# Kernel optimization log

Hardware: AMD Instinct MI355X
Metric: run time of the kernel (lower is better)

The kernel has to match this reference:

```python
import jax, jax.numpy as jnp
import numpy as np
from jax import lax

NEG = -1e30  # finite stand-in for -inf so logaddexp grads stay finite


def setup_inputs() -> dict:
    key = jax.random.key(0)
    k1, k2, k3, k4, k5 = jax.random.split(key, 5)
    B, T, L, S = 16, 2048, 256, 8
    return {
        "emissions": jax.random.normal(k1, (B, T, S), dtype=jnp.float32),
        "transition": jax.random.normal(k2, (S, S), dtype=jnp.float32),
        "bos": jax.random.normal(k3, (S,), dtype=jnp.float32),
        "eos": jax.random.normal(k4, (S,), dtype=jnp.float32),
        "lengths": jnp.full((B,), T, dtype=jnp.int32),
        "targets": jax.random.randint(k5, (B, L), 0, 4, dtype=jnp.int32),
        "target_lengths": jnp.full((B,), L, dtype=jnp.int32),
    }


def _den_logz(em, lengths, transition, bos, eos):
    # Exact log-semiring forward over the fully-connected 8-state denominator CRF graph
    # (the limit of k2.intersect_dense_pruned(...).get_tot_scores(log_semiring=True)).
    B, T, S = em.shape
    alpha0 = bos[None, :] + em[:, 0, :]  # (B,S)

    def step(alpha, em_t):
        a = jax.nn.logsumexp(alpha[:, :, None] + transition[None, :, :], axis=1) + em_t
        return a, a

    _, alphas = lax.scan(step, alpha0, jnp.swapaxes(em, 0, 1)[1:])  # (T-1,B,S)
    alphas = jnp.concatenate([alpha0[None], alphas], axis=0)  # (T,B,S)
    fin = alphas[lengths - 1, jnp.arange(B)]  # (B,S) alpha at last valid frame
    return jax.nn.logsumexp(fin + eos[None, :], axis=-1)


def _num_logz(em, lengths, targets, target_lengths, transition, bos, eos):
    # Forward over the target-constrained enter/extend lattice: symbol u must be
    # entered (state targets[u]) exactly once, optionally extended (state targets[u]+4),
    # then the path moves monotonically to symbol u+1.
    B, T, S = em.shape
    L = targets.shape[1]
    b_idx = jnp.arange(B)
    es = targets          # enter-state ids, (B,L)
    xs = targets + 4      # extend-state ids, (B,L)

    t_xx = transition[xs, xs]  # extend_u -> extend_u
    t_ex = transition[es, xs]  # enter_u  -> extend_u
    prev_e = jnp.concatenate([es[:, :1], es[:, :-1]], axis=1)
    prev_x = jnp.concatenate([xs[:, :1], xs[:, :-1]], axis=1)
    t_ee = transition[prev_e, es]  # enter_{u-1}  -> enter_u
    t_xe = transition[prev_x, es]  # extend_{u-1} -> enter_u

    a_e0 = jnp.full((B, L), NEG, dtype=em.dtype)
    a_e0 = a_e0.at[:, 0].set(bos[es[:, 0]] + em[b_idx, 0, es[:, 0]])
    a_x0 = jnp.full((B, L), NEG, dtype=em.dtype)

    def shift(a):  # a[:, u-1], NEG at u=0
        return jnp.concatenate([jnp.full((B, 1), NEG, dtype=a.dtype), a[:, :-1]], axis=1)

    def step(carry, em_t):
        a_e, a_x = carry
        em_e = jnp.take_along_axis(em_t, es, axis=1)  # (B,L)
        em_x = jnp.take_along_axis(em_t, xs, axis=1)
        new_e = em_e + jnp.logaddexp(shift(a_e) + t_ee, shift(a_x) + t_xe)
        new_x = em_x + jnp.logaddexp(a_e + t_ex, a_x + t_xx)
        return (new_e, new_x), (new_e, new_x)

    _, (ae, ax) = lax.scan(step, (a_e0, a_x0), jnp.swapaxes(em, 0, 1)[1:])
    ae = jnp.concatenate([a_e0[None], ae], axis=0)  # (T,B,L)
    ax = jnp.concatenate([a_x0[None], ax], axis=0)
    fin_e = ae[lengths - 1, b_idx]  # (B,L)
    fin_x = ax[lengths - 1, b_idx]
    u = target_lengths - 1
    fe = fin_e[b_idx, u] + eos[es[b_idx, u]]
    fx = fin_x[b_idx, u] + eos[xs[b_idx, u]]
    return jnp.logaddexp(fe, fx)  # (B,)


def reference(emissions, transition, bos, eos, lengths, targets, target_lengths):
    em = emissions.astype(jnp.float32)
    logz_den = _den_logz(em, lengths, transition, bos, eos)
    logz_num = _num_logz(em, lengths, targets, target_lengths, transition, bos, eos)
    # all samples valid by construction (lengths > 0, 0 < target_len <= length)
    return jnp.mean(logz_den - logz_num)
```

## Files before the change

### kernel.cpp

```cpp
#include <hip/hip_runtime.h>
#include <math.h>


#define LOG2E 1.4426950408889634f
#define LN2   0.69314718055994531f
#define CTL_WSHL1  0x130
#define CTL_WSHR1  0x138
#define CTL_ROR(r) (0x120 + (r))

#define AST(p, v) __hip_atomic_store((p), (v), __ATOMIC_RELAXED, __HIP_MEMORY_SCOPE_AGENT)
#define ALD(p)    __hip_atomic_load((p), __ATOMIC_RELAXED, __HIP_MEMORY_SCOPE_AGENT)

template <int CTRL>
__device__ __forceinline__ float fdpp(float x) {
    return __int_as_float(__builtin_amdgcn_update_dpp(
        0, __float_as_int(x), CTRL, 0xF, 0xF, true));
}
template <int CTRL>
__device__ __forceinline__ int idpp(int x) {
    return __builtin_amdgcn_update_dpp(0, x, CTRL, 0xF, 0xF, true);
}

__device__ __forceinline__ void pin() {
#if __has_builtin(__builtin_amdgcn_sched_barrier)
    __builtin_amdgcn_sched_barrier(0);
#else
    asm volatile("" ::: "memory");
#endif
}

__device__ __forceinline__ float fexp2(float x) {
#if __has_builtin(__builtin_amdgcn_exp2f)
    return __builtin_amdgcn_exp2f(x);
#else
    return exp2f(x);
#endif
}
__device__ __forceinline__ float flog2(float x) {
#if __has_builtin(__builtin_amdgcn_logf)
    return __builtin_amdgcn_logf(x);
#else
    return __log2f(x);
#endif
}
__device__ __forceinline__ float lse2(float a, float b) {
    float m = fmaxf(a, b);
    float d = fminf(a, b) - m;
    return m + flog2(1.0f + fexp2(d));
}

struct NumC { float tee[4], txe[4], tex[4], txx[4]; };

__device__ __forceinline__ void numf_step(const float2* p, float* E, float* X,
                                          float teeF, float txeF, const NumC& c) {
    float nbE = fdpp<CTL_WSHR1>(E[3]);
    float nbX = fdpp<CTL_WSHR1>(X[3]);
    float nE0 = p[0].x * fmaf(nbE,  teeF,     nbX  * txeF);
    float nE1 = p[1].x * fmaf(E[0], c.tee[1], X[0] * c.txe[1]);
    float nE2 = p[2].x * fmaf(E[1], c.tee[2], X[1] * c.txe[2]);
    float nE3 = p[3].x * fmaf(E[2], c.tee[3], X[2] * c.txe[3]);
    float nX0 = p[0].y * fmaf(E[0], c.tex[0], X[0] * c.txx[0]);
    float nX1 = p[1].y * fmaf(E[1], c.tex[1], X[1] * c.txx[1]);
    float nX2 = p[2].y * fmaf(E[2], c.tex[2], X[2] * c.txx[2]);
    float nX3 = p[3].y * fmaf(E[3], c.tex[3], X[3] * c.txx[3]);
    E[0] = nE0; E[1] = nE1; E[2] = nE2; E[3] = nE3;
    X[0] = nX0; X[1] = nX1; X[2] = nX2; X[3] = nX3;
}

__device__ __forceinline__ void numf_boundary(float* E, float* X, int& s,
                                              float& teeF, float& txeF,
                                              int lane, const NumC& c) {
    float m = fmaxf(fmaxf(fmaxf(E[0], E[1]), fmaxf(E[2], E[3])),
                    fmaxf(fmaxf(X[0], X[1]), fmaxf(X[2], X[3])));
    const bool live = (m > 0.0f);
    const int ex = live ? ((int)(__float_as_uint(m) >> 23) - 126) : 0;
    s += ex;
    const int bs = idpp<CTL_WSHR1>(s);
    if (!live) s = bs;
    int d = (lane == 0) ? 0 : (bs - s);
    const int extra = (d > 30) ? d : 0;
    s += extra; d -= extra;
    const float fsc = ldexpf(1.0f, -(ex + extra));
#pragma unroll
    for (int k = 0; k < 4; ++k) { E[k] *= fsc; X[k] *= fsc; }
    const float fs0 = (lane == 0) ? 0.0f : ldexpf(1.0f, d);
    teeF = c.tee[0] * fs0;
    txeF = c.txe[0] * fs0;
}

__device__ __forceinline__ void numb_step(const float2* p, float* bE, float* bX,
                                          const float* tex, const float* txx,
                                          const float* teeN, const float* txeN,
                                          float teeN3F, float txeN3F) {
    float mm0 = p[0].x * bE[0];
    float mm1 = p[1].x * bE[1];
    float mm2 = p[2].x * bE[2];
    float mm3 = p[3].x * bE[3];
    float m10 = p[0].y * bX[0];
    float m11 = p[1].y * bX[1];
    float m12 = p[2].y * bX[2];
    float m13 = p[3].y * bX[3];
    float mup = fdpp<CTL_WSHL1>(mm0);
    float nE0 = fmaf(tex[0], m10, teeN[0] * mm1);
    float nE1 = fmaf(tex[1], m11, teeN[1] * mm2);
    float nE2 = fmaf(tex[2], m12, teeN[2] * mm3);
    float nE3 = fmaf(tex[3], m13, teeN3F   * mup);
    float nX0 = fmaf(txx[0], m10, txeN[0] * mm1);
    float nX1 = fmaf(txx[1], m11, txeN[1] * mm2);
    float nX2 = fmaf(txx[2], m12, txeN[2] * mm3);
    float nX3 = fmaf(txx[3], m13, txeN3F   * mup);
    bE[0] = nE0; bE[1] = nE1; bE[2] = nE2; bE[3] = nE3;
    bX[0] = nX0; bX[1] = nX1; bX[2] = nX2; bX[3] = nX3;
}

__device__ __forceinline__ void numb_boundary(float* bE, float* bX, int& s,
                                              float& teeN3F, float& txeN3F,
                                              int lane, float teeN3, float txeN3) {
    float m = fmaxf(fmaxf(fmaxf(bE[0], bE[1]), fmaxf(bE[2], bE[3])),
                    fmaxf(fmaxf(bX[0], bX[1]), fmaxf(bX[2], bX[3])));
    const bool live = (m > 0.0f);
    const int ex = live ? ((int)(__float_as_uint(m) >> 23) - 126) : 0;
    s += ex;
    const int bs = idpp<CTL_WSHL1>(s);
    if (!live) s = bs;
    int d = (lane == 63) ? 0 : (bs - s);
    const int extra = (d > 30) ? d : 0;
    s += extra; d -= extra;
    const float fsc = ldexpf(1.0f, -(ex + extra));
#pragma unroll
    for (int k = 0; k < 4; ++k) { bE[k] *= fsc; bX[k] *= fsc; }
    const float fs = (lane == 63) ? 0.0f : ldexpf(1.0f, d);
    teeN3F = teeN3 * fs;
    txeN3F = txeN3 * fs;
}

__device__ __forceinline__ void steps4_fwd(const float4 buf[4][2], float* E, float* X,
                                           float teeF, float txeF, const NumC& c) {
#pragma unroll
    for (int q = 0; q < 4; ++q) {
        float2 p[4];
#pragma unroll
        for (int k = 0; k < 4; ++k) {
            const float4 v = buf[k][q >> 1];
            p[k] = (q & 1) ? make_float2(v.z, v.w) : make_float2(v.x, v.y);
        }
        numf_step(p, E, X, teeF, txeF, c);
    }
}
__device__ __forceinline__ void steps4_bwd(const float4 buf[4][2], float* bE, float* bX,
                                           const float* tex, const float* txx,
                                           const float* teeN, const float* txeN,
                                           float teeN3F, float txeN3F) {
#pragma unroll
    for (int q = 0; q < 4; ++q) {
        const int h = 1 - (q >> 1);
        float2 p[4];
#pragma unroll
        for (int k = 0; k < 4; ++k) {
            const float4 v = buf[k][h];
            p[k] = (q & 1) ? make_float2(v.x, v.y) : make_float2(v.z, v.w);
        }
        numb_step(p, bE, bX, tex, txx, teeN, txeN, teeN3F, txeN3F);
    }
}

__device__ __forceinline__ float denf_step(float al, float emt, const float* Tr) {
    float v1 = fdpp<CTL_ROR(1)>(al);
    float v2 = fdpp<CTL_ROR(2)>(al);
    float v3 = fdpp<CTL_ROR(3)>(al);
    float v4 = fdpp<CTL_ROR(4)>(al);
    float v5 = fdpp<CTL_ROR(5)>(al);
    float v6 = fdpp<CTL_ROR(6)>(al);
    float v7 = fdpp<CTL_ROR(7)>(al);
    float q0 = fmaf(v1, Tr[1], al * Tr[0]);
    float q1 = fmaf(v3, Tr[3], v2 * Tr[2]);
    float q2 = fmaf(v5, Tr[5], v4 * Tr[4]);
    float q3 = fmaf(v7, Tr[7], v6 * Tr[6]);
    return ((q0 + q1) + (q2 + q3)) * emt;
}
__device__ __forceinline__ float denb_step(float al, float emt, const float* TrB) {
    float g  = al * emt;
    float v1 = fdpp<CTL_ROR(7)>(g);
    float v2 = fdpp<CTL_ROR(6)>(g);
    float v3 = fdpp<CTL_ROR(5)>(g);
    float v4 = fdpp<CTL_ROR(4)>(g);
    float v5 = fdpp<CTL_ROR(3)>(g);
    float v6 = fdpp<CTL_ROR(2)>(g);
    float v7 = fdpp<CTL_ROR(1)>(g);
    float q0 = fmaf(v1, TrB[1], g * TrB[0]);
    float q1 = fmaf(v3, TrB[3], v2 * TrB[2]);
    float q2 = fmaf(v5, TrB[5], v4 * TrB[4]);
    float q3 = fmaf(v7, TrB[7], v6 * TrB[6]);
    return (q0 + q1) + (q2 + q3);
}
__device__ __forceinline__ int den_renorm(float& al) {
    float mm = fmaxf(al, fdpp<CTL_ROR(4)>(al));
    mm = fmaxf(mm, fdpp<CTL_ROR(2)>(mm));
    mm = fmaxf(mm, fdpp<CTL_ROR(1)>(mm));
    const int ex = (int)(__float_as_uint(mm) >> 23) - 126;
    al = ldexpf(al, -ex);
    return ex;
}

extern "C" __global__ void __launch_bounds__(128)
crf_fused(const float* __restrict__ em, const float* __restrict__ trans,
          const float* __restrict__ bos, const float* __restrict__ eos,
          const int* __restrict__ lengths, const int* __restrict__ targets,
          const int* __restrict__ tlens,
          float* __restrict__ ws, float* __restrict__ out,
          int B, int T, int S, int L)
{
    extern __shared__ float sm[];
    const int bid  = blockIdx.x;
    const int tid  = threadIdx.x;
    const int lane = tid & 63;
    const int wv   = tid >> 6;
    const int half = S >> 1;
    const int role = bid / B;
    const int b    = bid % B;
    const float* gem = em + (size_t)b * T * S;
    const int len = lengths[b];
    const int tm  = (len - 1) >> 1;
    const int P2  = T + 2;
    const int Th2 = P2 >> 1;

    float* NF  = ws + 16 + (size_t)b * 576;
    float* NB  = ws + 16 + (size_t)B * 576 + (size_t)b * 576;
    float* DEN = ws + 16 + (size_t)(2 * B) * 576;
    int* ticket = (int*)ws;

    if (role < 2) {
        float2* s2 = (float2*)sm;
        for (int t = tid; t < T; t += 128) {
            const float4* gr = (const float4*)(gem + t * S);
            float4 a = gr[0], c4 = gr[1];
            s2[0 * P2 + t] = make_float2(fexp2(a.x * LOG2E), fexp2(c4.x * LOG2E));
            s2[1 * P2 + t] = make_float2(fexp2(a.y * LOG2E), fexp2(c4.y * LOG2E));
            s2[2 * P2 + t] = make_float2(fexp2(a.z * LOG2E), fexp2(c4.z * LOG2E));
            s2[3 * P2 + t] = make_float2(fexp2(a.w * LOG2E), fexp2(c4.w * LOG2E));
        }
    } else {
        for (int t = tid; t < T; t += 128) {
            const float4* gr = (const float4*)(gem + t * S);
            float4 a = gr[0], c4 = gr[1];
            float4 w0, w1;
            w0.x = fexp2(a.x * LOG2E); w0.y = fexp2(c4.x * LOG2E);
            w0.z = fexp2(a.y * LOG2E); w0.w = fexp2(c4.y * LOG2E);
            w1.x = fexp2(a.z * LOG2E); w1.y = fexp2(c4.z * LOG2E);
            w1.z = fexp2(a.w * LOG2E); w1.w = fexp2(c4.w * LOG2E);
            ((float4*)sm)[t * 2]     = w0;
            ((float4*)sm)[t * 2 + 1] = w1;
        }
    }
    __syncthreads();

    if (role == 0 && wv == 0) {
        const float2* s2 = (const float2*)sm;
        const float4* s4 = (const float4*)sm;
        const int u0 = lane * 4;
        int e[4], ep[4];
        const int base = b * L;
#pragma unroll
        for (int k = 0; k < 4; ++k) {
            int u = u0 + k;
            e[k] = targets[base + ((u < L) ? u : (L - 1))];
        }
        ep[0] = (u0 > 0) ? targets[base + u0 - 1] : e[0];
        ep[1] = e[0]; ep[2] = e[1]; ep[3] = e[2];
        NumC c;
#pragma unroll
        for (int k = 0; k < 4; ++k) {
            c.tee[k] = fexp2(trans[ep[k] * S + e[k]] * LOG2E);
            c.txe[k] = fexp2(trans[(ep[k] + half) * S + e[k]] * LOG2E);
            c.tex[k] = fexp2(trans[e[k] * S + e[k] + half] * LOG2E);
            c.txx[k] = fexp2(trans[(e[k] + half) * S + e[k] + half] * LOG2E);
        }
        float E[4] = {0.f,0.f,0.f,0.f}, X[4] = {0.f,0.f,0.f,0.f};
        int s = 0;
        if (lane == 0) E[0] = fexp2(bos[e[0]] * LOG2E) * s2[e[0] * P2].x;
        float teeF = (lane == 0) ? 0.0f : c.tee[0];
        float txeF = (lane == 0) ? 0.0f : c.txe[0];

        int t0 = 1;
        while (t0 <= tm && (t0 & 1)) {
            float2 p[4];
#pragma unroll
            for (int k = 0; k < 4; ++k) p[k] = s2[e[k] * P2 + t0];
            numf_step(p, E, X, teeF, txeF, c);
            ++t0;
        }
        if (t0 + 7 <= tm) {
            float4 A[4][2], Bf[4][2];
#pragma unroll
            for (int k = 0; k < 4; ++k) {
                A[k][0] = s4[e[k] * Th2 + (t0 >> 1)];
                A[k][1] = s4[e[k] * Th2 + ((t0 + 2) >> 1)];
            }
            pin();
            while (t0 + 7 <= tm) {
#pragma unroll
                for (int k = 0; k < 4; ++k) {
                    Bf[k][0] = s4[e[k] * Th2 + ((t0 + 4) >> 1)];
                    Bf[k][1] = s4[e[k] * Th2 + ((t0 + 6) >> 1)];
                }
                pin();
                steps4_fwd(A, E, X, teeF, txeF, c);
#pragma unroll
                for (int k = 0; k < 4; ++k) {
                    A[k][0] = s4[e[k] * Th2 + ((t0 + 8) >> 1)];
                    A[k][1] = s4[e[k] * Th2 + ((t0 + 10) >> 1)];
                }
                pin();
                steps4_fwd(Bf, E, X, teeF, txeF, c);
                numf_boundary(E, X, s, teeF, txeF, lane, c);
                t0 += 8;
            }
        }
        while (t0 <= tm) {
            float2 p[4];
#pragma unroll
            for (int k = 0; k < 4; ++k) p[k] = s2[e[k] * P2 + t0];
            numf_step(p, E, X, teeF, txeF, c);
            ++t0;
        }
#pragma unroll
        for (int k = 0; k < 4; ++k) {
            AST(&NF[lane * 8 + k],     E[k]);
            AST(&NF[lane * 8 + 4 + k], X[k]);
        }
        AST(&NF[512 + lane], __int_as_float(s));
    } else if (role == 1 && wv == 0) {
        const float2* s2 = (const float2*)sm;
        const float4* s4 = (const float4*)sm;
        const int u0 = lane * 4;
        int e[5];
        const int base = b * L;
#pragma unroll
        for (int k = 0; k < 5; ++k) {
            int u = u0 + k;
            e[k] = targets[base + ((u < L) ? u : (L - 1))];
        }
        float tex[4], txx[4], teeN[4], txeN[4];
#pragma unroll
        for (int k = 0; k < 4; ++k) {
            tex[k]  = fexp2(trans[e[k] * S + e[k] + half] * LOG2E);
            txx[k]  = fexp2(trans[(e[k] + half) * S + e[k] + half] * LOG2E);
            teeN[k] = fexp2(trans[e[k] * S + e[k + 1]] * LOG2E);
            txeN[k] = fexp2(trans[(e[k] + half) * S + e[k + 1]] * LOG2E);
        }
        if (lane == 63) { teeN[3] = 0.0f; txeN[3] = 0.0f; }
        float bE[4] = {0.f,0.f,0.f,0.f}, bX[4] = {0.f,0.f,0.f,0.f};
        const int uf = tlens[b] - 1;
        if (lane == (uf >> 2)) {
            const int kf = uf & 3;
            bE[kf] = fexp2(eos[e[kf]] * LOG2E);
            bX[kf] = fexp2(eos[e[kf] + half] * LOG2E);
        }
        int s = 0;
        float teeN3F = teeN[3], txeN3F = txeN[3];

        int t1 = len - 1;
        const int tlo = tm + 1;
        while (t1 >= tlo && !(t1 & 1)) {
            float2 p[4];
#pragma unroll
            for (int k = 0; k < 4; ++k) p[k] = s2[e[k] * P2 + t1];
            numb_step(p, bE, bX, tex, txx, teeN, txeN, teeN3F, txeN3F);
            --t1;
        }
        if (t1 - 7 >= tlo) {
            float4 A[4][2], Bf[4][2];
#pragma unroll
            for (int k = 0; k < 4; ++k) {
                A[k][0] = s4[e[k] * Th2 + ((t1 - 3) >> 1)];
                A[k][1] = s4[e[k] * Th2 + ((t1 - 1) >> 1)];
            }
            pin();
            while (t1 - 7 >= tlo) {
#pragma unroll
                for (int k = 0; k < 4; ++k) {
                    Bf[k][0] = s4[e[k] * Th2 + ((t1 - 7) >> 1)];
                    Bf[k][1] = s4[e[k] * Th2 + ((t1 - 5) >> 1)];
                }
                pin();
                steps4_bwd(A, bE, bX, tex, txx, teeN, txeN, teeN3F, txeN3F);
                const int ta = (t1 - 11 > 0) ? (t1 - 11) : 0;
#pragma unroll
                for (int k = 0; k < 4; ++k) {
                    A[k][0] = s4[e[k] * Th2 + (ta >> 1)];
                    A[k][1] = s4[e[k] * Th2 + ((ta + 2) >> 1)];
                }
                pin();
                steps4_bwd(Bf, bE, bX, tex, txx, teeN, txeN, teeN3F, txeN3F);
                numb_boundary(bE, bX, s, teeN3F, txeN3F, lane, teeN[3], txeN[3]);
                t1 -= 8;
            }
        }
        while (t1 >= tlo) {
            float2 p[4];
#pragma unroll
            for (int k = 0; k < 4; ++k) p[k] = s2[e[k] * P2 + t1];
            numb_step(p, bE, bX, tex, txx, teeN, txeN, teeN3F, txeN3F);
            --t1;
        }
#pragma unroll
        for (int k = 0; k < 4; ++k) {
            AST(&NB[lane * 8 + k],     bE[k]);
            AST(&NB[lane * 8 + 4 + k], bX[k]);
        }
        AST(&NB[512 + lane], __int_as_float(s));
    } else if (role == 2) {
        float* denF  = sm + T * 8 + 16;
        float* denB  = denF + 8;
        int*   denFs = (int*)(denB + 8);
        int*   denBs = denFs + 8;
        const int j  = lane & 7;
        const int jj = ((j & 3) << 1) + (j >> 2);
        if (wv == 0) {
            float Tr[8];
#pragma unroll
            for (int r = 0; r < 8; ++r)
                Tr[r] = fexp2(trans[((j - r) & 7) * S + j] * LOG2E);
            float al = fexp2(bos[j] * LOG2E) * sm[jj];
            int sc = 0;
            int t = 1;
            while (t + 3 <= tm) {
                float c0 = sm[t * 8 + jj];
                float c1 = sm[(t + 1) * 8 + jj];
                float c2 = sm[(t + 2) * 8 + jj];
                float c3 = sm[(t + 3) * 8 + jj];
                pin();
                al = denf_step(al, c0, Tr);
                al = denf_step(al, c1, Tr);
                al = denf_step(al, c2, Tr);
                al = denf_step(al, c3, Tr);
                sc += den_renorm(al);
                t += 4;
            }
            while (t <= tm) { al = denf_step(al, sm[t * 8 + jj], Tr); ++t; }
            if (lane < 8) { denF[j] = al; denFs[j] = sc; }
        } else {
            float TrB[8];
#pragma unroll
            for (int r = 0; r < 8; ++r)
                TrB[r] = fexp2(trans[j * S + ((j + r) & 7)] * LOG2E);
            float al = fexp2(eos[j] * LOG2E);
            int sc = 0;
            int t = len - 1;
            const int tlo = tm + 1;
            while (t - 3 >= tlo) {
                float c0 = sm[t * 8 + jj];
                float c1 = sm[(t - 1) * 8 + jj];
                float c2 = sm[(t - 2) * 8 + jj];
                float c3 = sm[(t - 3) * 8 + jj];
                pin();
                al = denb_step(al, c0, TrB);
                al = denb_step(al, c1, TrB);
                al = denb_step(al, c2, TrB);
                al = denb_step(al, c3, TrB);
                sc += den_renorm(al);
                t -= 4;
            }
            while (t >= tlo) { al = denb_step(al, sm[t * 8 + jj], TrB); --t; }
            if (lane < 8) { denB[j] = al; denBs[j] = sc; }
        }
        __syncthreads();
        if (wv == 0 && lane < 8) {
            const float a  = fmaxf(denF[j], 1e-37f);
            const float bb = fmaxf(denB[j], 1e-37f);
            float part = flog2(a) + flog2(bb) + (float)(denFs[j] + denBs[j]);
            part = lse2(part, __shfl_xor(part, 1, 64));
            part = lse2(part, __shfl_xor(part, 2, 64));
            part = lse2(part, __shfl_xor(part, 4, 64));
            if (j == 0) AST(&DEN[b], part);
        }
    }

    __syncthreads();
    int* wflag = (int*)sm;
    if (tid == 0) {
        __threadfence();
        const int tk = atomicAdd(ticket, 1);
        wflag[0] = (tk == 3 * B - 1) ? 1 : 0;
    }
    __syncthreads();
    if (wflag[0] && tid < 64) {
        __threadfence();
        float acc = 0.0f;
        for (int bb2 = 0; bb2 < B; ++bb2) {
            const float* nf = ws + 16 + (size_t)bb2 * 576;
            const float* nb = ws + 16 + (size_t)B * 576 + (size_t)bb2 * 576;
            float v = 0.0f;
#pragma unroll
            for (int k = 0; k < 8; ++k)
                v = fmaf(ALD(&nf[lane * 8 + k]), ALD(&nb[lane * 8 + k]), v);
            const int st = __float_as_int(ALD(&nf[512 + lane]))
                         + __float_as_int(ALD(&nb[512 + lane]));
            float part = (v > 0.0f) ? (flog2(v) + (float)st) : -3.0e38f;
#pragma unroll
            for (int o = 1; o < 64; o <<= 1)
                part = lse2(part, __shfl_xor(part, o, 64));
            if (lane == 0) acc += ALD(&DEN[bb2]) - part;
        }
        if (lane == 0) out[0] = acc * (LN2 / (float)B);
    }
}

extern "C" void kernel_launch(void* const* d_in, const int* in_sizes, int n_in,
                              void* d_out, int out_size, void* d_ws, size_t ws_size,
                              hipStream_t stream)
{
    const float* em      = (const float*)d_in[0];
    const float* trans   = (const float*)d_in[1];
    const float* bos     = (const float*)d_in[2];
    const float* eos     = (const float*)d_in[3];
    const int*   lengths = (const int*)d_in[4];
    const int*   targets = (const int*)d_in[5];
    const int*   tlens   = (const int*)d_in[6];
    float* out = (float*)d_out;
    float* ws  = (float*)d_ws;

    const int B  = in_sizes[4];
    const int SS = in_sizes[1];
    int S = 1; while (S * S < SS) ++S;
    const int T = in_sizes[0] / (B * S);
    const int L = in_sizes[5] / B;

    const size_t shmem = (size_t)(T * 8 + 80) * sizeof(float);

    (void)hipMemsetAsync(ws, 0, 64, stream);
    hipLaunchKernelGGL(crf_fused, dim3(3 * B), dim3(128), shmem, stream,
                       em, trans, bos, eos, lengths, targets, tlens,
                       ws, out, B, T, S, L);
}
```

Before: 159.7 us.

## Pack all roles for two samples into one 512-thread block sharing emission LDS

Replaces the 3*B grid of 128-thread blocks (one role per block, each reloading and exponentiating the sample's emissions) with B/2 blocks of 512 threads. Each block holds two samples' exp-emissions in shared memory, and its eight waves run num-forward, num-backward, den-forward and den-backward for both samples. The denominator recursions now read the numerator's float2 layout and software-prefetch the next four frames. This removes the duplicated emission loading and exp work and the extra blocks, at the cost of larger LDS per block (raised via a function attribute) and fewer workgroups spread across CUs.

```diff
diff --git a/kernel.cpp b/kernel.cpp
--- a/kernel.cpp
+++ b/kernel.cpp
@@ -202,7 +202,7 @@
     return ex;
 }
 
-extern "C" __global__ void __launch_bounds__(128)
+extern "C" __global__ void __launch_bounds__(512)
 crf_fused(const float* __restrict__ em, const float* __restrict__ trans,
           const float* __restrict__ bos, const float* __restrict__ eos,
           const int* __restrict__ lengths, const int* __restrict__ targets,
@@ -216,47 +216,43 @@
     const int lane = tid & 63;
     const int wv   = tid >> 6;
     const int half = S >> 1;
-    const int role = bid / B;
-    const int b    = bid % B;
-    const float* gem = em + (size_t)b * T * S;
-    const int len = lengths[b];
-    const int tm  = (len - 1) >> 1;
-    const int P2  = T + 2;
-    const int Th2 = P2 >> 1;
+    const int role = wv >> 1;
+    const int smp  = wv & 1;
+    const int b    = 2 * bid + smp;
+    const int len  = lengths[(b < B) ? b : 0];
+    const int tm   = (len - 1) >> 1;
+    const int P2   = T + 2;
+    const int Th2  = P2 >> 1;
+    const int SPF  = 4 * P2;
 
     float* NF  = ws + 16 + (size_t)b * 576;
     float* NB  = ws + 16 + (size_t)B * 576 + (size_t)b * 576;
     float* DEN = ws + 16 + (size_t)(2 * B) * 576;
     int* ticket = (int*)ws;
 
-    if (role < 2) {
-        float2* s2 = (float2*)sm;
-        for (int t = tid; t < T; t += 128) {
-            const float4* gr = (const float4*)(gem + t * S);
+    {
+        float2* s2w = (float2*)sm;
+        const int nrows = (2 * bid + 2 <= B) ? 2 * T : T;
+        for (int i = tid; i < nrows; i += 512) {
+            const int si = (i >= T) ? 1 : 0;
+            const int t  = i - si * T;
+            const float4* gr =
+                (const float4*)(em + ((size_t)(2 * bid + si) * T + t) * S);
             float4 a = gr[0], c4 = gr[1];
-            s2[0 * P2 + t] = make_float2(fexp2(a.x * LOG2E), fexp2(c4.x * LOG2E));
-            s2[1 * P2 + t] = make_float2(fexp2(a.y * LOG2E), fexp2(c4.y * LOG2E));
-            s2[2 * P2 + t] = make_float2(fexp2(a.z * LOG2E), fexp2(c4.z * LOG2E));
-            s2[3 * P2 + t] = make_float2(fexp2(a.w * LOG2E), fexp2(c4.w * LOG2E));
-        }
-    } else {
-        for (int t = tid; t < T; t += 128) {
-            const float4* gr = (const float4*)(gem + t * S);
-            float4 a = gr[0], c4 = gr[1];
-            float4 w0, w1;
-            w0.x = fexp2(a.x * LOG2E); w0.y = fexp2(c4.x * LOG2E);
-            w0.z = fexp2(a.y * LOG2E); w0.w = fexp2(c4.y * LOG2E);
-            w1.x = fexp2(a.z * LOG2E); w1.y = fexp2(c4.z * LOG2E);
-            w1.z = fexp2(a.w * LOG2E); w1.w = fexp2(c4.w * LOG2E);
-            ((float4*)sm)[t * 2]     = w0;
-            ((float4*)sm)[t * 2 + 1] = w1;
+            float2* s2s = s2w + si * SPF;
+            s2s[0 * P2 + t] = make_float2(fexp2(a.x * LOG2E), fexp2(c4.x * LOG2E));
+            s2s[1 * P2 + t] = make_float2(fexp2(a.y * LOG2E), fexp2(c4.y * LOG2E));
+            s2s[2 * P2 + t] = make_float2(fexp2(a.z * LOG2E), fexp2(c4.z * LOG2E));
+            s2s[3 * P2 + t] = make_float2(fexp2(a.w * LOG2E), fexp2(c4.w * LOG2E));
         }
     }
     __syncthreads();
 
-    if (role == 0 && wv == 0) {
-        const float2* s2 = (const float2*)sm;
-        const float4* s4 = (const float4*)sm;
+    const float2* s2 = (const float2*)sm + smp * SPF;
+    const float4* s4 = (const float4*)sm + smp * (SPF >> 1);
+    float* scr = sm + 4 * SPF + smp * 32;
+
+    if (role == 0 && b < B) {
         const int u0 = lane * 4;
         int e[4], ep[4];
         const int base = b * L;
@@ -329,9 +325,7 @@
             AST(&NF[lane * 8 + 4 + k], X[k]);
         }
         AST(&NF[512 + lane], __int_as_float(s));
-    } else if (role == 1 && wv == 0) {
-        const float2* s2 = (const float2*)sm;
-        const float4* s4 = (const float4*)sm;
+    } else if (role == 1 && b < B) {
         const int u0 = lane * 4;
         int e[5];
         const int base = b * L;
@@ -409,71 +403,101 @@
             AST(&NB[lane * 8 + 4 + k], bX[k]);
         }
         AST(&NB[512 + lane], __int_as_float(s));
-    } else if (role == 2) {
-        float* denF  = sm + T * 8 + 16;
-        float* denB  = denF + 8;
-        int*   denFs = (int*)(denB + 8);
-        int*   denBs = denFs + 8;
+    } else if (role == 2 && b < B) {
         const int j  = lane & 7;
-        const int jj = ((j & 3) << 1) + (j >> 2);
-        if (wv == 0) {
-            float Tr[8];
-#pragma unroll
-            for (int r = 0; r < 8; ++r)
-                Tr[r] = fexp2(trans[((j - r) & 7) * S + j] * LOG2E);
-            float al = fexp2(bos[j] * LOG2E) * sm[jj];
-            int sc = 0;
-            int t = 1;
-            while (t + 3 <= tm) {
-                float c0 = sm[t * 8 + jj];
-                float c1 = sm[(t + 1) * 8 + jj];
-                float c2 = sm[(t + 2) * 8 + jj];
-                float c3 = sm[(t + 3) * 8 + jj];
+        const bool hi = (lane & 4) != 0;
+        const int rb = (j & 3) * P2;
+        float Tr[8];
+#pragma unroll
+        for (int r = 0; r < 8; ++r)
+            Tr[r] = fexp2(trans[((j - r) & 7) * S + j] * LOG2E);
+        const float2 c00 = s2[rb];
+        float al = fexp2(bos[j] * LOG2E) * (hi ? c00.y : c00.x);
+        int sc = 0;
+        int t = 1;
+        if (t + 3 <= tm) {
+            float2 a0 = s2[rb + t],     a1 = s2[rb + t + 1],
+                   a2 = s2[rb + t + 2], a3 = s2[rb + t + 3];
+            pin();
+            while (t + 7 <= tm) {
+                float2 b0 = s2[rb + t + 4], b1 = s2[rb + t + 5],
+                       b2 = s2[rb + t + 6], b3 = s2[rb + t + 7];
                 pin();
-                al = denf_step(al, c0, Tr);
-                al = denf_step(al, c1, Tr);
-                al = denf_step(al, c2, Tr);
-                al = denf_step(al, c3, Tr);
+                al = denf_step(al, hi ? a0.y : a0.x, Tr);
+                al = denf_step(al, hi ? a1.y : a1.x, Tr);
+                al = denf_step(al, hi ? a2.y : a2.x, Tr);
+                al = denf_step(al, hi ? a3.y : a3.x, Tr);
                 sc += den_renorm(al);
+                a0 = b0; a1 = b1; a2 = b2; a3 = b3;
                 t += 4;
             }
-            while (t <= tm) { al = denf_step(al, sm[t * 8 + jj], Tr); ++t; }
-            if (lane < 8) { denF[j] = al; denFs[j] = sc; }
-        } else {
-            float TrB[8];
-#pragma unroll
-            for (int r = 0; r < 8; ++r)
-                TrB[r] = fexp2(trans[j * S + ((j + r) & 7)] * LOG2E);
-            float al = fexp2(eos[j] * LOG2E);
-            int sc = 0;
-            int t = len - 1;
-            const int tlo = tm + 1;
-            while (t - 3 >= tlo) {
-                float c0 = sm[t * 8 + jj];
-                float c1 = sm[(t - 1) * 8 + jj];
-                float c2 = sm[(t - 2) * 8 + jj];
-                float c3 = sm[(t - 3) * 8 + jj];
+            al = denf_step(al, hi ? a0.y : a0.x, Tr);
+            al = denf_step(al, hi ? a1.y : a1.x, Tr);
+            al = denf_step(al, hi ? a2.y : a2.x, Tr);
+            al = denf_step(al, hi ? a3.y : a3.x, Tr);
+            sc += den_renorm(al);
+            t += 4;
+        }
+        while (t <= tm) {
+            float2 cc = s2[rb + t];
+            al = denf_step(al, hi ? cc.y : cc.x, Tr);
+            ++t;
+        }
+        if (lane < 8) { scr[j] = al; ((int*)scr)[16 + j] = sc; }
+    } else if (role == 3 && b < B) {
+        const int j  = lane & 7;
+        const bool hi = (lane & 4) != 0;
+        const int rb = (j & 3) * P2;
+        float TrB[8];
+#pragma unroll
+        for (int r = 0; r < 8; ++r)
+            TrB[r] = fexp2(trans[j * S + ((j + r) & 7)] * LOG2E);
+        float al = fexp2(eos[j] * LOG2E);
+        int sc = 0;
+        int t = len - 1;
+        const int tlo = tm + 1;
+        if (t - 3 >= tlo) {
+            float2 a0 = s2[rb + t],     a1 = s2[rb + t - 1],
+                   a2 = s2[rb + t - 2], a3 = s2[rb + t - 3];
+            pin();
+            while (t - 7 >= tlo) {
+                float2 b0 = s2[rb + t - 4], b1 = s2[rb + t - 5],
+                       b2 = s2[rb + t - 6], b3 = s2[rb + t - 7];
                 pin();
-                al = denb_step(al, c0, TrB);
-                al = denb_step(al, c1, TrB);
-                al = denb_step(al, c2, TrB);
-                al = denb_step(al, c3, TrB);
+                al = denb_step(al, hi ? a0.y : a0.x, TrB);
+                al = denb_step(al, hi ? a1.y : a1.x, TrB);
+                al = denb_step(al, hi ? a2.y : a2.x, TrB);
+                al = denb_step(al, hi ? a3.y : a3.x, TrB);
                 sc += den_renorm(al);
+                a0 = b0; a1 = b1; a2 = b2; a3 = b3;
                 t -= 4;
             }
-            while (t >= tlo) { al = denb_step(al, sm[t * 8 + jj], TrB); --t; }
-            if (lane < 8) { denB[j] = al; denBs[j] = sc; }
-        }
-        __syncthreads();
-        if (wv == 0 && lane < 8) {
-            const float a  = fmaxf(denF[j], 1e-37f);
-            const float bb = fmaxf(denB[j], 1e-37f);
-            float part = flog2(a) + flog2(bb) + (float)(denFs[j] + denBs[j]);
-            part = lse2(part, __shfl_xor(part, 1, 64));
-            part = lse2(part, __shfl_xor(part, 2, 64));
-            part = lse2(part, __shfl_xor(part, 4, 64));
-            if (j == 0) AST(&DEN[b], part);
-        }
+            al = denb_step(al, hi ? a0.y : a0.x, TrB);
+            al = denb_step(al, hi ? a1.y : a1.x, TrB);
+            al = denb_step(al, hi ? a2.y : a2.x, TrB);
+            al = denb_step(al, hi ? a3.y : a3.x, TrB);
+            sc += den_renorm(al);
+            t -= 4;
+        }
+        while (t >= tlo) {
+            float2 cc = s2[rb + t];
+            al = denb_step(al, hi ? cc.y : cc.x, TrB);
+            --t;
+        }
+        if (lane < 8) { scr[8 + j] = al; ((int*)scr)[24 + j] = sc; }
+    }
+
+    __syncthreads();
+    if (role == 2 && lane < 8 && b < B) {
+        const int j = lane;
+        const float a  = fmaxf(scr[j],     1e-37f);
+        const float bb = fmaxf(scr[8 + j], 1e-37f);
+        float part = flog2(a) + flog2(bb)
+                   + (float)(((int*)scr)[16 + j] + ((int*)scr)[24 + j]);
+        part = lse2(part, __shfl_xor(part, 1, 64));
+        part = lse2(part, __shfl_xor(part, 2, 64));
+        part = lse2(part, __shfl_xor(part, 4, 64));
+        if (j == 0) AST(&DEN[b], part);
     }
 
     __syncthreads();
@@ -481,7 +505,7 @@
     if (tid == 0) {
         __threadfence();
         const int tk = atomicAdd(ticket, 1);
-        wflag[0] = (tk == 3 * B - 1) ? 1 : 0;
+        wflag[0] = (tk == (int)gridDim.x - 1) ? 1 : 0;
     }
     __syncthreads();
     if (wflag[0] && tid < 64) {
@@ -526,10 +550,19 @@
     const int T = in_sizes[0] / (B * S);
     const int L = in_sizes[5] / B;
 
-    const size_t shmem = (size_t)(T * 8 + 80) * sizeof(float);
+    const int nblk = (B + 1) / 2;
+    const size_t shmem = (size_t)(16 * (T + 2) + 96) * sizeof(float);
+
+    static bool attr_done = false;
+    if (!attr_done) {
+        (void)hipFuncSetAttribute((const void*)crf_fused,
+                                  hipFuncAttributeMaxDynamicSharedMemorySize,
+                                  (int)(140 * 1024));
+        attr_done = true;
+    }
 
     (void)hipMemsetAsync(ws, 0, 64, stream);
-    hipLaunchKernelGGL(crf_fused, dim3(3 * B), dim3(128), shmem, stream,
+    hipLaunchKernelGGL(crf_fused, dim3(nblk), dim3(512), shmem, stream,
                        em, trans, bos, eos, lengths, targets, tlens,
                        ws, out, B, T, S, L);
 }
```

Result: slower. 193.0 us (+20.9%).

## Double-buffer 8-step LDS windows in numerator and software-pipeline denominator loads

Applied to the files above, without the earlier changes.

The numerator forward and backward scans now load whole 8-step windows from LDS into two register buffers (U/V), so the next window's loads are issued while the current window is computed, replacing the earlier half-window prefetch scheme. The denominator scans prefetch the next four emission values before computing the current four. A few independent statements are reordered so the boundary-lane terms start earlier, and the max dynamic shared memory attribute is set once. This hides LDS latency on the serial recurrence at the cost of more registers, which could reduce occupancy or cause spills.

```diff
diff --git a/kernel.cpp b/kernel.cpp
--- a/kernel.cpp
+++ b/kernel.cpp
@@ -55,14 +55,14 @@
                                           float teeF, float txeF, const NumC& c) {
     float nbE = fdpp<CTL_WSHR1>(E[3]);
     float nbX = fdpp<CTL_WSHR1>(X[3]);
+    float nE3 = p[3].x * fmaf(E[2], c.tee[3], X[2] * c.txe[3]);
+    float nX3 = p[3].y * fmaf(E[3], c.tex[3], X[3] * c.txx[3]);
     float nE0 = p[0].x * fmaf(nbE,  teeF,     nbX  * txeF);
     float nE1 = p[1].x * fmaf(E[0], c.tee[1], X[0] * c.txe[1]);
     float nE2 = p[2].x * fmaf(E[1], c.tee[2], X[1] * c.txe[2]);
-    float nE3 = p[3].x * fmaf(E[2], c.tee[3], X[2] * c.txe[3]);
     float nX0 = p[0].y * fmaf(E[0], c.tex[0], X[0] * c.txx[0]);
     float nX1 = p[1].y * fmaf(E[1], c.tex[1], X[1] * c.txx[1]);
     float nX2 = p[2].y * fmaf(E[2], c.tex[2], X[2] * c.txx[2]);
-    float nX3 = p[3].y * fmaf(E[3], c.tex[3], X[3] * c.txx[3]);
     E[0] = nE0; E[1] = nE1; E[2] = nE2; E[3] = nE3;
     X[0] = nX0; X[1] = nX1; X[2] = nX2; X[3] = nX3;
 }
@@ -102,10 +102,10 @@
     float m13 = p[3].y * bX[3];
     float mup = fdpp<CTL_WSHL1>(mm0);
     float nE0 = fmaf(tex[0], m10, teeN[0] * mm1);
+    float nX0 = fmaf(txx[0], m10, txeN[0] * mm1);
     float nE1 = fmaf(tex[1], m11, teeN[1] * mm2);
     float nE2 = fmaf(tex[2], m12, teeN[2] * mm3);
     float nE3 = fmaf(tex[3], m13, teeN3F   * mup);
-    float nX0 = fmaf(txx[0], m10, txeN[0] * mm1);
     float nX1 = fmaf(txx[1], m11, txeN[1] * mm2);
     float nX2 = fmaf(txx[2], m12, txeN[2] * mm3);
     float nX3 = fmaf(txx[3], m13, txeN3F   * mup);
@@ -161,6 +161,41 @@
             p[k] = (q & 1) ? make_float2(v.x, v.y) : make_float2(v.z, v.w);
         }
         numb_step(p, bE, bX, tex, txx, teeN, txeN, teeN3F, txeN3F);
+    }
+}
+
+__device__ __forceinline__ void win8_fwd(const float4 (&buf)[4][4], float* E, float* X,
+                                         int& s, float& teeF, float& txeF,
+                                         int lane, const NumC& c) {
+    float4 h[4][2];
+#pragma unroll
+    for (int k = 0; k < 4; ++k) { h[k][0] = buf[k][0]; h[k][1] = buf[k][1]; }
+    steps4_fwd(h, E, X, teeF, txeF, c);
+#pragma unroll
+    for (int k = 0; k < 4; ++k) { h[k][0] = buf[k][2]; h[k][1] = buf[k][3]; }
+    steps4_fwd(h, E, X, teeF, txeF, c);
+    numf_boundary(E, X, s, teeF, txeF, lane, c);
+}
+__device__ __forceinline__ void win8_bwd(const float4 (&buf)[4][4], float* bE, float* bX,
+                                         int& s, float& teeN3F, float& txeN3F, int lane,
+                                         const float* tex, const float* txx,
+                                         const float* teeN, const float* txeN,
+                                         float teeN3, float txeN3) {
+    float4 h[4][2];
+#pragma unroll
+    for (int k = 0; k < 4; ++k) { h[k][0] = buf[k][2]; h[k][1] = buf[k][3]; }
+    steps4_bwd(h, bE, bX, tex, txx, teeN, txeN, teeN3F, txeN3F);
+#pragma unroll
+    for (int k = 0; k < 4; ++k) { h[k][0] = buf[k][0]; h[k][1] = buf[k][1]; }
+    steps4_bwd(h, bE, bX, tex, txx, teeN, txeN, teeN3F, txeN3F);
+    numb_boundary(bE, bX, s, teeN3F, txeN3F, lane, teeN3, txeN3);
+}
+
+__device__ __forceinline__ void loadw(float4 (&D)[4][4], const float4* const (&p)[4]) {
+#pragma unroll
+    for (int k = 0; k < 4; ++k) {
+#pragma unroll
+        for (int j = 0; j < 4; ++j) D[k][j] = p[k][j];
     }
 }
 
@@ -289,32 +324,42 @@
             numf_step(p, E, X, teeF, txeF, c);
             ++t0;
         }
-        if (t0 + 7 <= tm) {
-            float4 A[4][2], Bf[4][2];
+        const int nw = (t0 <= tm) ? ((tm - t0 + 1) >> 3) : 0;
+        if (nw >= 2) {
+            const float4* pf[4];
+#pragma unroll
+            for (int k = 0; k < 4; ++k) pf[k] = s4 + e[k] * Th2 + (t0 >> 1);
+            float4 U[4][4], V[4][4];
+            loadw(U, pf);
+#pragma unroll
+            for (int k = 0; k < 4; ++k) pf[k] += 4;
+            pin();
+            const int di = nw >> 1;
+            for (int i = 0; i < di; ++i) {
+                loadw(V, pf);
+#pragma unroll
+                for (int k = 0; k < 4; ++k) pf[k] += 4;
+                pin();
+                win8_fwd(U, E, X, s, teeF, txeF, lane, c);
+                loadw(U, pf);
+#pragma unroll
+                for (int k = 0; k < 4; ++k) pf[k] += 4;
+                pin();
+                win8_fwd(V, E, X, s, teeF, txeF, lane, c);
+                t0 += 16;
+            }
+        }
+        while (t0 + 7 <= tm) {
+            float4 D[4][4];
 #pragma unroll
             for (int k = 0; k < 4; ++k) {
-                A[k][0] = s4[e[k] * Th2 + (t0 >> 1)];
-                A[k][1] = s4[e[k] * Th2 + ((t0 + 2) >> 1)];
+                const float4* q = s4 + e[k] * Th2 + (t0 >> 1);
+#pragma unroll
+                for (int j = 0; j < 4; ++j) D[k][j] = q[j];
             }
             pin();
-            while (t0 + 7 <= tm) {
-#pragma unroll
-                for (int k = 0; k < 4; ++k) {
-                    Bf[k][0] = s4[e[k] * Th2 + ((t0 + 4) >> 1)];
-                    Bf[k][1] = s4[e[k] * Th2 + ((t0 + 6) >> 1)];
-                }
-                pin();
-                steps4_fwd(A, E, X, teeF, txeF, c);
-#pragma unroll
-                for (int k = 0; k < 4; ++k) {
-                    A[k][0] = s4[e[k] * Th2 + ((t0 + 8) >> 1)];
-                    A[k][1] = s4[e[k] * Th2 + ((t0 + 10) >> 1)];
-                }
-                pin();
-                steps4_fwd(Bf, E, X, teeF, txeF, c);
-                numf_boundary(E, X, s, teeF, txeF, lane, c);
-                t0 += 8;
-            }
+            win8_fwd(D, E, X, s, teeF, txeF, lane, c);
+            t0 += 8;
         }
         while (t0 <= tm) {
             float2 p[4];
@@ -368,33 +413,45 @@
             numb_step(p, bE, bX, tex, txx, teeN, txeN, teeN3F, txeN3F);
             --t1;
         }
-        if (t1 - 7 >= tlo) {
-            float4 A[4][2], Bf[4][2];
+        const int nw = (t1 >= tlo) ? ((t1 - tlo + 1) >> 3) : 0;
+        if (nw >= 2 && tlo >= 16) {
+            const float4* pb[4];
+#pragma unroll
+            for (int k = 0; k < 4; ++k) pb[k] = s4 + e[k] * Th2 + ((t1 - 7) >> 1);
+            float4 U[4][4], V[4][4];
+            loadw(U, pb);
+#pragma unroll
+            for (int k = 0; k < 4; ++k) pb[k] -= 4;
+            pin();
+            const int di = nw >> 1;
+            for (int i = 0; i < di; ++i) {
+                loadw(V, pb);
+#pragma unroll
+                for (int k = 0; k < 4; ++k) pb[k] -= 4;
+                pin();
+                win8_bwd(U, bE, bX, s, teeN3F, txeN3F, lane,
+                         tex, txx, teeN, txeN, teeN[3], txeN[3]);
+                loadw(U, pb);
+#pragma unroll
+                for (int k = 0; k < 4; ++k) pb[k] -= 4;
+                pin();
+                win8_bwd(V, bE, bX, s, teeN3F, txeN3F, lane,
+                         tex, txx, teeN, txeN, teeN[3], txeN[3]);
+                t1 -= 16;
+            }
+        }
+        while (t1 - 7 >= tlo) {
+            float4 D[4][4];
 #pragma unroll
             for (int k = 0; k < 4; ++k) {
-                A[k][0] = s4[e[k] * Th2 + ((t1 - 3) >> 1)];
-                A[k][1] = s4[e[k] * Th2 + ((t1 - 1) >> 1)];
+                const float4* q = s4 + e[k] * Th2 + ((t1 - 7) >> 1);
+#pragma unroll
+                for (int j = 0; j < 4; ++j) D[k][j] = q[j];
             }
             pin();
-            while (t1 - 7 >= tlo) {
-#pragma unroll
-                for (int k = 0; k < 4; ++k) {
-                    Bf[k][0] = s4[e[k] * Th2 + ((t1 - 7) >> 1)];
-                    Bf[k][1] = s4[e[k] * Th2 + ((t1 - 5) >> 1)];
-                }
-                pin();
-                steps4_bwd(A, bE, bX, tex, txx, teeN, txeN, teeN3F, txeN3F);
-                const int ta = (t1 - 11 > 0) ? (t1 - 11) : 0;
-#pragma unroll
-                for (int k = 0; k < 4; ++k) {
-                    A[k][0] = s4[e[k] * Th2 + (ta >> 1)];
-                    A[k][1] = s4[e[k] * Th2 + ((ta + 2) >> 1)];
-                }
-                pin();
-                steps4_bwd(Bf, bE, bX, tex, txx, teeN, txeN, teeN3F, txeN3F);
-                numb_boundary(bE, bX, s, teeN3F, txeN3F, lane, teeN[3], txeN[3]);
-                t1 -= 8;
-            }
+            win8_bwd(D, bE, bX, s, teeN3F, txeN3F, lane,
+                     tex, txx, teeN, txeN, teeN[3], txeN[3]);
+            t1 -= 8;
         }
         while (t1 >= tlo) {
             float2 p[4];
@@ -424,12 +481,26 @@
             float al = fexp2(bos[j] * LOG2E) * sm[jj];
             int sc = 0;
             int t = 1;
-            while (t + 3 <= tm) {
+            if (t + 3 <= tm) {
                 float c0 = sm[t * 8 + jj];
                 float c1 = sm[(t + 1) * 8 + jj];
                 float c2 = sm[(t + 2) * 8 + jj];
                 float c3 = sm[(t + 3) * 8 + jj];
                 pin();
+                while (t + 7 <= tm) {
+                    float d0 = sm[(t + 4) * 8 + jj];
+                    float d1 = sm[(t + 5) * 8 + jj];
+                    float d2 = sm[(t + 6) * 8 + jj];
+                    float d3 = sm[(t + 7) * 8 + jj];
+                    pin();
+                    al = denf_step(al, c0, Tr);
+                    al = denf_step(al, c1, Tr);
+                    al = denf_step(al, c2, Tr);
+                    al = denf_step(al, c3, Tr);
+                    sc += den_renorm(al);
+                    c0 = d0; c1 = d1; c2 = d2; c3 = d3;
+                    t += 4;
+                }
                 al = denf_step(al, c0, Tr);
                 al = denf_step(al, c1, Tr);
                 al = denf_step(al, c2, Tr);
@@ -448,12 +519,26 @@
             int sc = 0;
             int t = len - 1;
             const int tlo = tm + 1;
-            while (t - 3 >= tlo) {
+            if (t - 3 >= tlo) {
                 float c0 = sm[t * 8 + jj];
                 float c1 = sm[(t - 1) * 8 + jj];
                 float c2 = sm[(t - 2) * 8 + jj];
                 float c3 = sm[(t - 3) * 8 + jj];
                 pin();
+                while (t - 7 >= tlo) {
+                    float d0 = sm[(t - 4) * 8 + jj];
+                    float d1 = sm[(t - 5) * 8 + jj];
+                    float d2 = sm[(t - 6) * 8 + jj];
+                    float d3 = sm[(t - 7) * 8 + jj];
+                    pin();
+                    al = denb_step(al, c0, TrB);
+                    al = denb_step(al, c1, TrB);
+                    al = denb_step(al, c2, TrB);
+                    al = denb_step(al, c3, TrB);
+                    sc += den_renorm(al);
+                    c0 = d0; c1 = d1; c2 = d2; c3 = d3;
+                    t -= 4;
+                }
                 al = denb_step(al, c0, TrB);
                 al = denb_step(al, c1, TrB);
                 al = denb_step(al, c2, TrB);
@@ -528,6 +613,14 @@
 
     const size_t shmem = (size_t)(T * 8 + 80) * sizeof(float);
 
+    static bool attr_done = false;
+    if (!attr_done) {
+        (void)hipFuncSetAttribute((const void*)crf_fused,
+                                  hipFuncAttributeMaxDynamicSharedMemorySize,
+                                  (int)(96 * 1024));
+        attr_done = true;
+    }
+
     (void)hipMemsetAsync(ws, 0, 64, stream);
     hipLaunchKernelGGL(crf_fused, dim3(3 * B), dim3(128), shmem, stream,
                        em, trans, bos, eos, lengths, targets, tlens,
```

Measured after the change: 155.6 us. 1.03x faster.
